# Kernel optimization log

Measured on AMD Instinct MI355X. Metric: run time of the kernel, lower is better.

## Reference

```python
import jax, jax.numpy as jnp
import numpy as np

D_MODEL = 1024
D_FF = 4096
BATCH = 4
SEQ = 2048
DECAY = 0.9
THRESH = 0.5


def setup_inputs() -> dict:
    key = jax.random.key(0)
    k1, k2, k3, k4 = jax.random.split(key, 4)
    spikes = jax.random.normal(k1, (BATCH, SEQ, D_MODEL), dtype=jnp.float32)
    # xavier-ish init scales matching gains 0.5/0.5/0.3 in the torch module
    s1 = 0.5 * np.sqrt(2.0 / (D_MODEL + D_FF))
    s2 = 0.5 * np.sqrt(2.0 / (D_MODEL + D_FF))
    sr = 0.3 * np.sqrt(2.0 / (D_MODEL + D_FF))
    W1 = jax.random.normal(k2, (D_FF, D_MODEL), dtype=jnp.float32) * s1
    W2 = jax.random.normal(k3, (D_MODEL, D_FF), dtype=jnp.float32) * s2
    Wr = jax.random.normal(k4, (D_FF, D_MODEL), dtype=jnp.float32) * sr
    return {"spikes": spikes, "W1": W1, "W2": W2, "Wr": Wr}


def reference(spikes, W1, W2, Wr):
    # spikes: [B, T, D]; W1, Wr: [F, D]; W2: [D, F]
    B, T, D = spikes.shape
    F = W1.shape[0]
    d = jnp.float32(DECAY)
    one_minus_d = jnp.float32(1.0 - DECAY)
    # Hoist time-independent projections out of the recurrence (same math as
    # the per-timestep nn.Linear calls in the torch loop).
    r_all = jax.nn.sigmoid(jnp.einsum('btd,fd->btf', spikes, Wr))  # [B,T,F]
    h_all = jnp.einsum('btd,fd->btf', spikes, W1)                   # [B,T,F]

    def step(carry, xs):
        act, rec = carry              # [B,F] each, init zeros (fresh buffers)
        r_t, h_t = xs                 # [B,F]
        rec = d * rec + one_minus_d * r_t                 # mixed receptance
        mixed = d * act + one_minus_d * h_t               # temporal state mix
        spike = (mixed > THRESH).astype(h_t.dtype)        # eval-mode spikes
        gated = spike * r_t
        # torch detaches current_activation each step
        return (jax.lax.stop_gradient(mixed), rec), gated

    init = (jnp.zeros((B, F), spikes.dtype), jnp.zeros((B, F), spikes.dtype))
    _, gated = jax.lax.scan(step,
                            init,
                            (jnp.swapaxes(r_all, 0, 1), jnp.swapaxes(h_all, 0, 1)))
    # gated: [T, B, F] -> output [B, T, D]
    out = jnp.einsum('tbf,df->btd', gated, W2)
    return out
```

## Files before the change

### kernel.cpp

```cpp
#include <hip/hip_runtime.h>
#include <math.h>

#define B_    4
#define T_    2048
#define D_    1024
#define F_    4096
#define R_    (B_*T_)
#define SEG_  64
#define L_    (T_/SEG_)
#define DECAYF 0.9f
#define OMDF   0.1f
#define FLAG_THRESH 0.45f

typedef __attribute__((ext_vector_type(4)))  int   i32x4;
typedef __attribute__((ext_vector_type(8)))  int   i32x8;
typedef __attribute__((ext_vector_type(16))) float f32x16;

__device__ __forceinline__ int pk_fp8x4(float x, float y, float z, float w) {
    int p = 0;
    p = __builtin_amdgcn_cvt_pk_fp8_f32(x, y, p, false);
    p = __builtin_amdgcn_cvt_pk_fp8_f32(z, w, p, true);
    return p;
}

__device__ __forceinline__ size_t pk_off(int row, int d) {
    return ((size_t)((row >> 5) * 16 + (d >> 6)) * 2048)
         + ((d >> 4) & 1) * 1024
         + ((row & 31) + ((d >> 5) & 1) * 32) * 16
         + (d & 15);
}

#define KA_W1_BLOCKS  4096
#define KA_SEG_BLOCKS 256
#define KA_FLAG_BLOCKS 32

__global__ __launch_bounds__(256)
void kA_prologue(const float* __restrict__ spikes,
                 const float* __restrict__ W1,
                 unsigned char* __restrict__ w_f8,
                 float* __restrict__ seg_sum,
                 unsigned int* __restrict__ flags) {
    const int bid = blockIdx.x;
    const int tid = threadIdx.x;
    if (bid < KA_W1_BLOCKS) {
        int i = bid * 256 + tid;
        float4 v = ((const float4*)W1)[i];
        int f  = i >> 8;
        int d0 = (i & 255) * 4;
        *(int*)(w_f8 + pk_off(f, d0)) = pk_fp8x4(8.f*v.x, 8.f*v.y, 8.f*v.z, 8.f*v.w);
    } else if (bid < KA_W1_BLOCKS + KA_SEG_BLOCKS) {
        int t = (bid - KA_W1_BLOCKS) * 256 + tid;
        int dg = t & (D_ / 4 - 1);
        int s = (t >> 8) & (SEG_ - 1);
        int b = t >> 14;
        const float4* sp4 = (const float4*)spikes;
        const int base = (b * T_ + s * L_) * (D_ / 4) + dg;
        float4 e = {0.f, 0.f, 0.f, 0.f};
#pragma unroll 8
        for (int k = 0; k < L_; ++k) {
            float4 x = sp4[base + k * (D_ / 4)];
            e.x = DECAYF * e.x + OMDF * x.x;
            e.y = DECAYF * e.y + OMDF * x.y;
            e.z = DECAYF * e.z + OMDF * x.z;
            e.w = DECAYF * e.w + OMDF * x.w;
        }
        ((float4*)seg_sum)[(b * SEG_ + s) * (D_ / 4) + dg] = e;
    } else {
        int i = (bid - KA_W1_BLOCKS - KA_SEG_BLOCKS) * 256 + tid;
        if (i < R_) flags[i] = 0u;
    }
}

__global__ __launch_bounds__(256)
void kB_seg_scan(const float* __restrict__ seg_sum,
                 float* __restrict__ start_state) {
    int g = blockIdx.x * 256 + threadIdx.x;
    int s = g & 63;
    int c = g >> 6;
    int d = c & (D_ - 1);
    int b = c >> 10;
    int idx = (b * SEG_ + s) * D_ + d;
    float v = seg_sum[idx];
    float wp = 0.0343368382f;
#pragma unroll
    for (int off = 1; off < SEG_; off <<= 1) {
        float u = __shfl_up(v, off, 64);
        if (s >= off) v += wp * u;
        wp *= wp;
    }
    float pv = __shfl_up(v, 1, 64);
    start_state[idx] = (s == 0) ? 0.f : pv;
}

__global__ __launch_bounds__(256)
void kC_ema_fp8(const float* __restrict__ spikes,
                const float* __restrict__ start_state,
                unsigned char* __restrict__ a_f8) {
    int t = blockIdx.x * 256 + threadIdx.x;
    int dg = t & (D_ / 4 - 1);
    int s = (t >> 8) & (SEG_ - 1);
    int b = t >> 14;
    const float4* sp4 = (const float4*)spikes;
    const int base = (b * T_ + s * L_) * (D_ / 4) + dg;
    const int d0 = dg * 4;
    unsigned char* dst = a_f8 + pk_off(b * T_ + s * L_, d0);
    float4 e = ((const float4*)start_state)[(b * SEG_ + s) * (D_ / 4) + dg];
#pragma unroll 8
    for (int k = 0; k < L_; ++k) {
        float4 x = sp4[base + k * (D_ / 4)];
        e.x = DECAYF * e.x + OMDF * x.x;
        e.y = DECAYF * e.y + OMDF * x.y;
        e.z = DECAYF * e.z + OMDF * x.z;
        e.w = DECAYF * e.w + OMDF * x.w;
        *(int*)(dst + k * 16) = pk_fp8x4(8.f*e.x, 8.f*e.y, 8.f*e.z, 8.f*e.w);
    }
}

__global__ __launch_bounds__(256)
void k2_mfma_flags(const unsigned char* __restrict__ Ap,
                   const unsigned char* __restrict__ Bp,
                   unsigned int* __restrict__ flags) {
    const int tid = threadIdx.x;
    const int w = tid >> 6;
    const int lane = tid & 63;
    const int m0 = blockIdx.y * 128;
    const int n0 = blockIdx.x * 128;
    const int wm = w >> 1, wn = w & 1;
    const int kg = lane >> 5;

    const unsigned char* a0 = Ap + ((size_t)((m0 >> 5) + wm * 2 + 0) * 16) * 2048 + lane * 16;
    const unsigned char* a1 = Ap + ((size_t)((m0 >> 5) + wm * 2 + 1) * 16) * 2048 + lane * 16;
    const unsigned char* b0 = Bp + ((size_t)((n0 >> 5) + wn * 2 + 0) * 16) * 2048 + lane * 16;
    const unsigned char* b1 = Bp + ((size_t)((n0 >> 5) + wn * 2 + 1) * 16) * 2048 + lane * 16;

    f32x16 acc[2][2] = {};

#define LDFRAG(p, C)                                                        \
    ({ i32x4 lo_ = *(const i32x4*)((p) + (size_t)(C) * 2048);               \
       i32x4 hi_ = *(const i32x4*)((p) + (size_t)(C) * 2048 + 1024);        \
       (i32x8){lo_.x, lo_.y, lo_.z, lo_.w, hi_.x, hi_.y, hi_.z, hi_.w}; })

#define MFMA4(AF0, AF1, BF0, BF1)                                           \
    {                                                                       \
        acc[0][0] = __builtin_amdgcn_mfma_scale_f32_32x32x64_f8f6f4(        \
            AF0, BF0, acc[0][0], 0, 0, 0, 124, 0, 124);                     \
        acc[0][1] = __builtin_amdgcn_mfma_scale_f32_32x32x64_f8f6f4(        \
            AF0, BF1, acc[0][1], 0, 0, 0, 124, 0, 124);                     \
        acc[1][0] = __builtin_amdgcn_mfma_scale_f32_32x32x64_f8f6f4(        \
            AF1, BF0, acc[1][0], 0, 0, 0, 124, 0, 124);                     \
        acc[1][1] = __builtin_amdgcn_mfma_scale_f32_32x32x64_f8f6f4(        \
            AF1, BF1, acc[1][1], 0, 0, 0, 124, 0, 124);                     \
    }

    i32x8 A0a = LDFRAG(a0, 0), A1a = LDFRAG(a1, 0);
    i32x8 B0a = LDFRAG(b0, 0), B1a = LDFRAG(b1, 0);
#pragma unroll
    for (int C = 0; C < 16; C += 2) {
        i32x8 A0b = LDFRAG(a0, C + 1), A1b = LDFRAG(a1, C + 1);
        i32x8 B0b = LDFRAG(b0, C + 1), B1b = LDFRAG(b1, C + 1);
        MFMA4(A0a, A1a, B0a, B1a);
        const int C2 = (C + 2) & 15;
        A0a = LDFRAG(a0, C2); A1a = LDFRAG(a1, C2);
        B0a = LDFRAG(b0, C2); B1a = LDFRAG(b1, C2);
        MFMA4(A0b, A1b, B0b, B1b);
    }
#undef LDFRAG
#undef MFMA4

#pragma unroll
    for (int i = 0; i < 2; ++i) {
#pragma unroll
        for (int reg = 0; reg < 16; ++reg) {
            float mx = fmaxf(acc[i][0][reg], acc[i][1][reg]);
            if (mx > FLAG_THRESH) {
                const int rr = (reg & 3) + 8 * (reg >> 2) + 4 * kg;
                atomicOr(&flags[m0 + wm * 64 + i * 32 + rr], 1u);
            }
        }
    }
}

__global__ __launch_bounds__(256)
void k4_output(const float* __restrict__ spikes,
               const float* __restrict__ start_state,
               const float* __restrict__ W1,
               const float* __restrict__ Wr,
               const float* __restrict__ W2,
               const unsigned int* __restrict__ flags,
               float* __restrict__ out) {
    const int row = blockIdx.x;
    const int tid = threadIdx.x;
    float4 o = {0.f, 0.f, 0.f, 0.f};

    if (flags[row] == 0u) {
        *(float4*)&out[(size_t)row * D_ + tid * 4] = o;
        return;
    }

    __shared__ float se[D_];
    __shared__ float sp[D_];
    __shared__ float red[256];
    __shared__ int nspk;
    __shared__ int spk_list[256];

    const int b = row / T_;
    const int t = row % T_;
    const int seg = t / L_;
    const int off = t % L_;
    const int segbase = (b * T_ + seg * L_) * D_;

    for (int i = tid; i < D_; i += 256) {
        float e = start_state[(b * SEG_ + seg) * D_ + i];
        for (int j = 0; j <= off; ++j)
            e = DECAYF * e + OMDF * spikes[segbase + j * D_ + i];
        se[i] = e;
        sp[i] = spikes[(size_t)row * D_ + i];
    }
    if (tid == 0) nspk = 0;
    __syncthreads();

    for (int f0 = 0; f0 < F_; f0 += 256) {
        int f = f0 + tid;
        float mix = 0.f;
        for (int k = 0; k < D_; ++k) mix += se[k] * W1[(size_t)f * D_ + k];
        if (mix > 0.5f) {
            int idx = atomicAdd(&nspk, 1);
            spk_list[idx] = f;
        }
        __syncthreads();
        int n = nspk;
        for (int i = 0; i < n; ++i) {
            int fs = spk_list[i];
            float part = 0.f;
#pragma unroll
            for (int k = 0; k < 4; ++k)
                part += sp[tid * 4 + k] * Wr[(size_t)fs * D_ + tid * 4 + k];
            red[tid] = part;
            __syncthreads();
            for (int sft = 128; sft > 0; sft >>= 1) {
                if (tid < sft) red[tid] += red[tid + sft];
                __syncthreads();
            }
            float r = 1.f / (1.f + expf(-red[0]));
            __syncthreads();
            o.x += r * W2[(size_t)(tid * 4 + 0) * F_ + fs];
            o.y += r * W2[(size_t)(tid * 4 + 1) * F_ + fs];
            o.z += r * W2[(size_t)(tid * 4 + 2) * F_ + fs];
            o.w += r * W2[(size_t)(tid * 4 + 3) * F_ + fs];
        }
        __syncthreads();
        if (tid == 0) nspk = 0;
        __syncthreads();
    }
    *(float4*)&out[(size_t)row * D_ + tid * 4] = o;
}

extern "C" void kernel_launch(void* const* d_in, const int* in_sizes, int n_in,
                              void* d_out, int out_size, void* d_ws, size_t ws_size,
                              hipStream_t stream) {
    const float* spikes = (const float*)d_in[0];
    const float* W1     = (const float*)d_in[1];
    const float* W2     = (const float*)d_in[2];
    const float* Wr     = (const float*)d_in[3];
    float* out = (float*)d_out;

    char* ws = (char*)d_ws;
    float* seg_sum      = (float*)ws;
    float* start_state  = seg_sum + (size_t)B_ * SEG_ * D_;
    unsigned int* flags = (unsigned int*)(start_state + (size_t)B_ * SEG_ * D_);
    unsigned char* a_f8 = (unsigned char*)(flags + R_);
    unsigned char* w_f8 = a_f8 + (size_t)R_ * D_;

    kA_prologue<<<KA_W1_BLOCKS + KA_SEG_BLOCKS + KA_FLAG_BLOCKS, 256, 0, stream>>>(
        spikes, W1, w_f8, seg_sum, flags);
    kB_seg_scan<<<(B_ * D_ * 64) / 256, 256, 0, stream>>>(seg_sum, start_state);
    kC_ema_fp8<<<(B_ * SEG_ * D_ / 4) / 256, 256, 0, stream>>>(spikes, start_state, a_f8);

    dim3 g2(F_ / 128, R_ / 128);
    k2_mfma_flags<<<g2, 256, 0, stream>>>(a_f8, w_f8, flags);

    k4_output<<<R_, 256, 0, stream>>>(spikes, start_state, W1, Wr, W2, flags, out);
}
```

Baseline: 186.7 us.

## Swizzle GEMM tile order across XCDs and deepen register prefetch to four stages

```diff
diff --git a/kernel.cpp b/kernel.cpp
--- a/kernel.cpp
+++ b/kernel.cpp
@@ -123,8 +123,10 @@
     const int tid = threadIdx.x;
     const int w = tid >> 6;
     const int lane = tid & 63;
-    const int m0 = blockIdx.y * 128;
-    const int n0 = blockIdx.x * 128;
+    const int orig = blockIdx.x;
+    const int swz  = (orig & 7) * 256 + (orig >> 3);
+    const int m0 = (swz >> 5) * 128;
+    const int n0 = (swz & 31) * 128;
     const int wm = w >> 1, wn = w & 1;
     const int kg = lane >> 5;
 
@@ -135,9 +137,9 @@
 
     f32x16 acc[2][2] = {};
 
-#define LDFRAG(p, C)                                                        \
-    ({ i32x4 lo_ = *(const i32x4*)((p) + (size_t)(C) * 2048);               \
-       i32x4 hi_ = *(const i32x4*)((p) + (size_t)(C) * 2048 + 1024);        \
+#define LDF(p, OFF)                                                         \
+    ({ i32x4 lo_ = *(const i32x4*)((p) + (OFF));                            \
+       i32x4 hi_ = *(const i32x4*)((p) + (OFF) + 1024);                     \
        (i32x8){lo_.x, lo_.y, lo_.z, lo_.w, hi_.x, hi_.y, hi_.z, hi_.w}; })
 
 #define MFMA4(AF0, AF1, BF0, BF1)                                           \
@@ -152,19 +154,36 @@
             AF1, BF1, acc[1][1], 0, 0, 0, 124, 0, 124);                     \
     }
 
-    i32x8 A0a = LDFRAG(a0, 0), A1a = LDFRAG(a1, 0);
-    i32x8 B0a = LDFRAG(b0, 0), B1a = LDFRAG(b1, 0);
-#pragma unroll
-    for (int C = 0; C < 16; C += 2) {
-        i32x8 A0b = LDFRAG(a0, C + 1), A1b = LDFRAG(a1, C + 1);
-        i32x8 B0b = LDFRAG(b0, C + 1), B1b = LDFRAG(b1, C + 1);
-        MFMA4(A0a, A1a, B0a, B1a);
-        const int C2 = (C + 2) & 15;
-        A0a = LDFRAG(a0, C2); A1a = LDFRAG(a1, C2);
-        B0a = LDFRAG(b0, C2); B1a = LDFRAG(b1, C2);
-        MFMA4(A0b, A1b, B0b, B1b);
-    }
-#undef LDFRAG
+    i32x8 A0s0 = LDF(a0, 0),    A1s0 = LDF(a1, 0);
+    i32x8 B0s0 = LDF(b0, 0),    B1s0 = LDF(b1, 0);
+    i32x8 A0s1 = LDF(a0, 2048), A1s1 = LDF(a1, 2048);
+    i32x8 B0s1 = LDF(b0, 2048), B1s1 = LDF(b1, 2048);
+    i32x8 A0s2 = LDF(a0, 4096), A1s2 = LDF(a1, 4096);
+    i32x8 B0s2 = LDF(b0, 4096), B1s2 = LDF(b1, 4096);
+    i32x8 A0s3 = LDF(a0, 6144), A1s3 = LDF(a1, 6144);
+    i32x8 B0s3 = LDF(b0, 6144), B1s3 = LDF(b1, 6144);
+
+#pragma unroll 1
+    for (int p = 0; p < 3; ++p) {
+        const size_t off = (size_t)(p + 1) * 8192;
+        MFMA4(A0s0, A1s0, B0s0, B1s0);
+        A0s0 = LDF(a0, off);        A1s0 = LDF(a1, off);
+        B0s0 = LDF(b0, off);        B1s0 = LDF(b1, off);
+        MFMA4(A0s1, A1s1, B0s1, B1s1);
+        A0s1 = LDF(a0, off + 2048); A1s1 = LDF(a1, off + 2048);
+        B0s1 = LDF(b0, off + 2048); B1s1 = LDF(b1, off + 2048);
+        MFMA4(A0s2, A1s2, B0s2, B1s2);
+        A0s2 = LDF(a0, off + 4096); A1s2 = LDF(a1, off + 4096);
+        B0s2 = LDF(b0, off + 4096); B1s2 = LDF(b1, off + 4096);
+        MFMA4(A0s3, A1s3, B0s3, B1s3);
+        A0s3 = LDF(a0, off + 6144); A1s3 = LDF(a1, off + 6144);
+        B0s3 = LDF(b0, off + 6144); B1s3 = LDF(b1, off + 6144);
+    }
+    MFMA4(A0s0, A1s0, B0s0, B1s0);
+    MFMA4(A0s1, A1s1, B0s1, B1s1);
+    MFMA4(A0s2, A1s2, B0s2, B1s2);
+    MFMA4(A0s3, A1s3, B0s3, B1s3);
+#undef LDF
 #undef MFMA4
 
 #pragma unroll
@@ -276,8 +295,7 @@
     kB_seg_scan<<<(B_ * D_ * 64) / 256, 256, 0, stream>>>(seg_sum, start_state);
     kC_ema_fp8<<<(B_ * SEG_ * D_ / 4) / 256, 256, 0, stream>>>(spikes, start_state, a_f8);
 
-    dim3 g2(F_ / 128, R_ / 128);
-    k2_mfma_flags<<<g2, 256, 0, stream>>>(a_f8, w_f8, flags);
+    k2_mfma_flags<<<(R_ / 128) * (F_ / 128), 256, 0, stream>>>(a_f8, w_f8, flags);
 
     k4_output<<<R_, 256, 0, stream>>>(spikes, start_state, W1, Wr, W2, flags, out);
 }
```

Result: faster. 175.7 us (median of 2 runs) (-5.9%).

## Fuse segment scan into EMA kernel and widen FP8 MFMA tiles with XCD-aware mapping

Applied to the files above, without the earlier changes.

```diff
diff --git a/kernel.cpp b/kernel.cpp
--- a/kernel.cpp
+++ b/kernel.cpp
@@ -72,39 +72,31 @@
 }
 
 __global__ __launch_bounds__(256)
-void kB_seg_scan(const float* __restrict__ seg_sum,
-                 float* __restrict__ start_state) {
-    int g = blockIdx.x * 256 + threadIdx.x;
-    int s = g & 63;
-    int c = g >> 6;
-    int d = c & (D_ - 1);
-    int b = c >> 10;
-    int idx = (b * SEG_ + s) * D_ + d;
-    float v = seg_sum[idx];
-    float wp = 0.0343368382f;
-#pragma unroll
-    for (int off = 1; off < SEG_; off <<= 1) {
-        float u = __shfl_up(v, off, 64);
-        if (s >= off) v += wp * u;
-        wp *= wp;
-    }
-    float pv = __shfl_up(v, 1, 64);
-    start_state[idx] = (s == 0) ? 0.f : pv;
-}
-
-__global__ __launch_bounds__(256)
-void kC_ema_fp8(const float* __restrict__ spikes,
-                const float* __restrict__ start_state,
-                unsigned char* __restrict__ a_f8) {
+void kC_scan_ema_fp8(const float* __restrict__ spikes,
+                     const float* __restrict__ seg_sum,
+                     float* __restrict__ start_state,
+                     unsigned char* __restrict__ a_f8) {
     int t = blockIdx.x * 256 + threadIdx.x;
     int dg = t & (D_ / 4 - 1);
     int s = (t >> 8) & (SEG_ - 1);
     int b = t >> 14;
+
+    const float4* ss4 = (const float4*)seg_sum;
+    const float W = 0.0343368382f;
+    float4 e = {0.f, 0.f, 0.f, 0.f};
+    for (int j = 0; j < s; ++j) {
+        float4 g = ss4[(b * SEG_ + j) * (D_ / 4) + dg];
+        e.x = W * e.x + g.x;
+        e.y = W * e.y + g.y;
+        e.z = W * e.z + g.z;
+        e.w = W * e.w + g.w;
+    }
+    ((float4*)start_state)[(b * SEG_ + s) * (D_ / 4) + dg] = e;
+
     const float4* sp4 = (const float4*)spikes;
     const int base = (b * T_ + s * L_) * (D_ / 4) + dg;
     const int d0 = dg * 4;
     unsigned char* dst = a_f8 + pk_off(b * T_ + s * L_, d0);
-    float4 e = ((const float4*)start_state)[(b * SEG_ + s) * (D_ / 4) + dg];
 #pragma unroll 8
     for (int k = 0; k < L_; ++k) {
         float4 x = sp4[base + k * (D_ / 4)];
@@ -123,55 +115,53 @@
     const int tid = threadIdx.x;
     const int w = tid >> 6;
     const int lane = tid & 63;
-    const int m0 = blockIdx.y * 128;
-    const int n0 = blockIdx.x * 128;
+    const int orig = blockIdx.x;
+    const int xcd  = orig & 7;
+    const int id   = orig >> 3;
+    const int mt   = (xcd >> 1) * 16 + (id >> 3);
+    const int nt   = (xcd & 1) * 8 + (id & 7);
+    const int m0 = mt * 128;
+    const int n0 = nt * 256;
     const int wm = w >> 1, wn = w & 1;
     const int kg = lane >> 5;
 
-    const unsigned char* a0 = Ap + ((size_t)((m0 >> 5) + wm * 2 + 0) * 16) * 2048 + lane * 16;
-    const unsigned char* a1 = Ap + ((size_t)((m0 >> 5) + wm * 2 + 1) * 16) * 2048 + lane * 16;
-    const unsigned char* b0 = Bp + ((size_t)((n0 >> 5) + wn * 2 + 0) * 16) * 2048 + lane * 16;
-    const unsigned char* b1 = Bp + ((size_t)((n0 >> 5) + wn * 2 + 1) * 16) * 2048 + lane * 16;
-
-    f32x16 acc[2][2] = {};
+    const unsigned char* pA0 = Ap + ((size_t)((m0 >> 5) + wm * 2 + 0) * 16) * 2048 + lane * 16;
+    const unsigned char* pA1 = Ap + ((size_t)((m0 >> 5) + wm * 2 + 1) * 16) * 2048 + lane * 16;
+    const unsigned char* pB0 = Bp + ((size_t)((n0 >> 5) + wn * 4 + 0) * 16) * 2048 + lane * 16;
+    const unsigned char* pB1 = Bp + ((size_t)((n0 >> 5) + wn * 4 + 1) * 16) * 2048 + lane * 16;
+    const unsigned char* pB2 = Bp + ((size_t)((n0 >> 5) + wn * 4 + 2) * 16) * 2048 + lane * 16;
+    const unsigned char* pB3 = Bp + ((size_t)((n0 >> 5) + wn * 4 + 3) * 16) * 2048 + lane * 16;
+
+    f32x16 acc[2][4] = {};
 
 #define LDFRAG(p, C)                                                        \
     ({ i32x4 lo_ = *(const i32x4*)((p) + (size_t)(C) * 2048);               \
        i32x4 hi_ = *(const i32x4*)((p) + (size_t)(C) * 2048 + 1024);        \
        (i32x8){lo_.x, lo_.y, lo_.z, lo_.w, hi_.x, hi_.y, hi_.z, hi_.w}; })
 
-#define MFMA4(AF0, AF1, BF0, BF1)                                           \
-    {                                                                       \
-        acc[0][0] = __builtin_amdgcn_mfma_scale_f32_32x32x64_f8f6f4(        \
-            AF0, BF0, acc[0][0], 0, 0, 0, 124, 0, 124);                     \
-        acc[0][1] = __builtin_amdgcn_mfma_scale_f32_32x32x64_f8f6f4(        \
-            AF0, BF1, acc[0][1], 0, 0, 0, 124, 0, 124);                     \
-        acc[1][0] = __builtin_amdgcn_mfma_scale_f32_32x32x64_f8f6f4(        \
-            AF1, BF0, acc[1][0], 0, 0, 0, 124, 0, 124);                     \
-        acc[1][1] = __builtin_amdgcn_mfma_scale_f32_32x32x64_f8f6f4(        \
-            AF1, BF1, acc[1][1], 0, 0, 0, 124, 0, 124);                     \
-    }
-
-    i32x8 A0a = LDFRAG(a0, 0), A1a = LDFRAG(a1, 0);
-    i32x8 B0a = LDFRAG(b0, 0), B1a = LDFRAG(b1, 0);
-#pragma unroll
-    for (int C = 0; C < 16; C += 2) {
-        i32x8 A0b = LDFRAG(a0, C + 1), A1b = LDFRAG(a1, C + 1);
-        i32x8 B0b = LDFRAG(b0, C + 1), B1b = LDFRAG(b1, C + 1);
-        MFMA4(A0a, A1a, B0a, B1a);
-        const int C2 = (C + 2) & 15;
-        A0a = LDFRAG(a0, C2); A1a = LDFRAG(a1, C2);
-        B0a = LDFRAG(b0, C2); B1a = LDFRAG(b1, C2);
-        MFMA4(A0b, A1b, B0b, B1b);
+#define MFMA1(i, j, AF, BF)                                                 \
+    acc[i][j] = __builtin_amdgcn_mfma_scale_f32_32x32x64_f8f6f4(            \
+        AF, BF, acc[i][j], 0, 0, 0, 124, 0, 124);
+
+#pragma unroll
+    for (int C = 0; C < 16; ++C) {
+        i32x8 A0 = LDFRAG(pA0, C), A1 = LDFRAG(pA1, C);
+        i32x8 B0 = LDFRAG(pB0, C), B1 = LDFRAG(pB1, C);
+        i32x8 B2 = LDFRAG(pB2, C), B3 = LDFRAG(pB3, C);
+        MFMA1(0, 0, A0, B0) MFMA1(0, 1, A0, B1)
+        MFMA1(0, 2, A0, B2) MFMA1(0, 3, A0, B3)
+        MFMA1(1, 0, A1, B0) MFMA1(1, 1, A1, B1)
+        MFMA1(1, 2, A1, B2) MFMA1(1, 3, A1, B3)
     }
 #undef LDFRAG
-#undef MFMA4
+#undef MFMA1
 
 #pragma unroll
     for (int i = 0; i < 2; ++i) {
 #pragma unroll
         for (int reg = 0; reg < 16; ++reg) {
-            float mx = fmaxf(acc[i][0][reg], acc[i][1][reg]);
+            float mx = fmaxf(fmaxf(acc[i][0][reg], acc[i][1][reg]),
+                             fmaxf(acc[i][2][reg], acc[i][3][reg]));
             if (mx > FLAG_THRESH) {
                 const int rr = (reg & 3) + 8 * (reg >> 2) + 4 * kg;
                 atomicOr(&flags[m0 + wm * 64 + i * 32 + rr], 1u);
@@ -273,11 +263,11 @@
 
     kA_prologue<<<KA_W1_BLOCKS + KA_SEG_BLOCKS + KA_FLAG_BLOCKS, 256, 0, stream>>>(
         spikes, W1, w_f8, seg_sum, flags);
-    kB_seg_scan<<<(B_ * D_ * 64) / 256, 256, 0, stream>>>(seg_sum, start_state);
-    kC_ema_fp8<<<(B_ * SEG_ * D_ / 4) / 256, 256, 0, stream>>>(spikes, start_state, a_f8);
-
-    dim3 g2(F_ / 128, R_ / 128);
-    k2_mfma_flags<<<g2, 256, 0, stream>>>(a_f8, w_f8, flags);
+
+    kC_scan_ema_fp8<<<(B_ * SEG_ * D_ / 4) / 256, 256, 0, stream>>>(
+        spikes, seg_sum, start_state, a_f8);
+
+    k2_mfma_flags<<<(R_ / 128) * (F_ / 256), 256, 0, stream>>>(a_f8, w_f8, flags);
 
     k4_output<<<R_, 256, 0, stream>>>(spikes, start_state, W1, Wr, W2, flags, out);
 }
```

After: 265.4 us. 1.42x slower.

## Remap GEMM tiles per XCD and sync waves each K-chunk for cache reuse

Applied to the files above, without the earlier changes.

```diff
diff --git a/kernel.cpp b/kernel.cpp
--- a/kernel.cpp
+++ b/kernel.cpp
@@ -123,15 +123,20 @@
     const int tid = threadIdx.x;
     const int w = tid >> 6;
     const int lane = tid & 63;
-    const int m0 = blockIdx.y * 128;
-    const int n0 = blockIdx.x * 128;
+    const int orig = blockIdx.x;
+    const int xcd  = orig & 7;
+    const int id   = orig >> 3;
+    const int mt   = (xcd >> 1) * 16 + (id >> 4);
+    const int nt   = (xcd & 1) * 16 + (id & 15);
+    const int m0 = mt * 128;
+    const int n0 = nt * 128;
     const int wm = w >> 1, wn = w & 1;
     const int kg = lane >> 5;
 
-    const unsigned char* a0 = Ap + ((size_t)((m0 >> 5) + wm * 2 + 0) * 16) * 2048 + lane * 16;
-    const unsigned char* a1 = Ap + ((size_t)((m0 >> 5) + wm * 2 + 1) * 16) * 2048 + lane * 16;
-    const unsigned char* b0 = Bp + ((size_t)((n0 >> 5) + wn * 2 + 0) * 16) * 2048 + lane * 16;
-    const unsigned char* b1 = Bp + ((size_t)((n0 >> 5) + wn * 2 + 1) * 16) * 2048 + lane * 16;
+    const unsigned char* pa0 = Ap + ((size_t)((m0 >> 5) + wm * 2 + 0) * 16) * 2048 + lane * 16;
+    const unsigned char* pa1 = Ap + ((size_t)((m0 >> 5) + wm * 2 + 1) * 16) * 2048 + lane * 16;
+    const unsigned char* pb0 = Bp + ((size_t)((n0 >> 5) + wn * 2 + 0) * 16) * 2048 + lane * 16;
+    const unsigned char* pb1 = Bp + ((size_t)((n0 >> 5) + wn * 2 + 1) * 16) * 2048 + lane * 16;
 
     f32x16 acc[2][2] = {};
 
@@ -152,17 +157,13 @@
             AF1, BF1, acc[1][1], 0, 0, 0, 124, 0, 124);                     \
     }
 
-    i32x8 A0a = LDFRAG(a0, 0), A1a = LDFRAG(a1, 0);
-    i32x8 B0a = LDFRAG(b0, 0), B1a = LDFRAG(b1, 0);
-#pragma unroll
-    for (int C = 0; C < 16; C += 2) {
-        i32x8 A0b = LDFRAG(a0, C + 1), A1b = LDFRAG(a1, C + 1);
-        i32x8 B0b = LDFRAG(b0, C + 1), B1b = LDFRAG(b1, C + 1);
-        MFMA4(A0a, A1a, B0a, B1a);
-        const int C2 = (C + 2) & 15;
-        A0a = LDFRAG(a0, C2); A1a = LDFRAG(a1, C2);
-        B0a = LDFRAG(b0, C2); B1a = LDFRAG(b1, C2);
-        MFMA4(A0b, A1b, B0b, B1b);
+#pragma unroll
+    for (int C = 0; C < 16; ++C) {
+        __syncthreads();
+        __builtin_amdgcn_sched_barrier(0);
+        i32x8 A0 = LDFRAG(pa0, C), A1 = LDFRAG(pa1, C);
+        i32x8 B0 = LDFRAG(pb0, C), B1 = LDFRAG(pb1, C);
+        MFMA4(A0, A1, B0, B1);
     }
 #undef LDFRAG
 #undef MFMA4
@@ -276,8 +277,7 @@
     kB_seg_scan<<<(B_ * D_ * 64) / 256, 256, 0, stream>>>(seg_sum, start_state);
     kC_ema_fp8<<<(B_ * SEG_ * D_ / 4) / 256, 256, 0, stream>>>(spikes, start_state, a_f8);
 
-    dim3 g2(F_ / 128, R_ / 128);
-    k2_mfma_flags<<<g2, 256, 0, stream>>>(a_f8, w_f8, flags);
+    k2_mfma_flags<<<(R_ / 128) * (F_ / 128), 256, 0, stream>>>(a_f8, w_f8, flags);
 
     k4_output<<<R_, 256, 0, stream>>>(spikes, start_state, W1, Wr, W2, flags, out);
 }
```

Result: slower. 202.9 us (+8.7%).
